# Kernel tuning notes

Hardware: AMD Instinct MI355X
Metric: run time of the kernel (lower is better)

The kernel has to match this reference:

```python
import jax, jax.numpy as jnp
import numpy as np

B, S, D, H, DH = 2, 2048, 1024, 16, 64
GLOBAL_RATIO = 0.1
LN_EPS = 1e-5


def setup_inputs() -> dict:
    key = jax.random.key(0)
    ks = jax.random.split(key, 8)
    w = lambda k, shape: jax.random.normal(k, shape, jnp.float32) * 0.02
    return {
        'x': jax.random.normal(ks[0], (B, S, D), jnp.float32),
        'Wq': w(ks[1], (D, H * DH)),
        'Wk': w(ks[2], (D, H * DH)),
        'Wv': w(ks[3], (D, H * DH)),
        'Wo': w(ks[4], (H * DH, D)),
        'bo': jnp.zeros((D,), jnp.float32),
        'ln_gamma': jnp.ones((DH,), jnp.float32),
        'ln_beta': jnp.zeros((DH,), jnp.float32),
        'Wg': w(ks[5], (2 * DH, DH)),
        'bg': jnp.zeros((DH,), jnp.float32),
    }


def _layernorm(x, gamma, beta):
    mu = jnp.mean(x, axis=-1, keepdims=True)
    var = jnp.mean(jnp.square(x - mu), axis=-1, keepdims=True)
    return (x - mu) * jax.lax.rsqrt(var + LN_EPS) * gamma + beta


def reference(x, Wq, Wk, Wv, Wo, bo, ln_gamma, ln_beta, Wg, bg):
    b, s, _ = x.shape
    # projections -> [b, h, n, d]
    split = lambda t: t.reshape(b, s, H, DH).transpose(0, 2, 1, 3)
    q = split(x @ Wq)
    k = split(x @ Wk)
    v = split(x @ Wv)
    scale = DH ** -0.5

    # local (full) attention: manual QK^T / softmax / AV
    scores = jnp.einsum('bhnd,bhmd->bhnm', q, k) * scale  # [b,h,s,s]
    attn = jax.nn.softmax(scores, axis=-1)
    local_out = jnp.einsum('bhnm,bhmd->bhnd', attn, v)

    # cross-segment fusion: top-k keys by norm per (b, h)
    num_global = max(1, int(s * GLOBAL_RATIO))
    key_norms = jnp.linalg.norm(k, axis=-1)  # [b,h,s]
    _, top_idx = jax.lax.top_k(key_norms, num_global)  # [b,h,g]
    idx = top_idx[..., None]  # [b,h,g,1]
    global_k = jnp.take_along_axis(k, idx, axis=2)  # [b,h,g,d]
    global_v = jnp.take_along_axis(v, idx, axis=2)
    g_scores = jnp.einsum('bhnd,bhgd->bhng', q, global_k) * scale
    g_attn = jax.nn.softmax(g_scores, axis=-1)
    global_out = jnp.einsum('bhng,bhgd->bhnd', g_attn, global_v)
    global_out = _layernorm(global_out, ln_gamma, ln_beta)

    # learned gate over [local, global]
    cat = jnp.concatenate([local_out, global_out], axis=-1)  # [b,h,s,2d]
    gate = jax.nn.sigmoid(cat @ Wg + bg)
    fused = gate * local_out + (1.0 - gate) * global_out

    out = fused.transpose(0, 2, 1, 3).reshape(b, s, H * DH)  # b h n d -> b n (h d)
    return out @ Wo + bo
```

## Files before the change

### kernel.cpp

```cpp
#include <hip/hip_runtime.h>


constexpr int SEQ    = 2048;
constexpr int DMODEL = 1024;
constexpr int NH     = 16;
constexpr int DHEAD  = 64;
constexpr int BHT    = 32;
constexpr int NG     = 204;
constexpr int NGPAD  = 256;
constexpr float LNEPS = 1e-5f;

typedef __attribute__((ext_vector_type(8))) short short8;
typedef __attribute__((ext_vector_type(4))) short short4v;
typedef __attribute__((ext_vector_type(4))) float f32x4;

__device__ __forceinline__ unsigned short f2bf(float f) {
    unsigned int u = __float_as_uint(f);
    u += 0x7FFFu + ((u >> 16) & 1u);
    return (unsigned short)(u >> 16);
}
__device__ __forceinline__ float bf2f(unsigned short b) {
    return __uint_as_float(((unsigned int)b) << 16);
}

__global__ __launch_bounds__(256)
void prep_k(const float* __restrict__ x,
            const float* __restrict__ Wq, const float* __restrict__ Wv,
            const float* __restrict__ Wo, const float* __restrict__ Wk,
            const float* __restrict__ Wg,
            unsigned short* __restrict__ xh, unsigned short* __restrict__ xl,
            unsigned short* __restrict__ Wqt, unsigned short* __restrict__ Wvt,
            unsigned short* __restrict__ Wot, unsigned short* __restrict__ Wkh,
            unsigned short* __restrict__ Wkl, unsigned short* __restrict__ Wgt)
{
    const int bid = blockIdx.x;
    const int tid = threadIdx.x;

    if (bid < 2048) {
        int i = (bid * 256 + tid) << 3;
        short8 h, l;
#pragma unroll
        for (int j = 0; j < 8; ++j) {
            float v = x[i + j];
            unsigned short hb = f2bf(v);
            h[j] = (short)hb;
            l[j] = (short)f2bf(v - bf2f(hb));
        }
        *(short8*)(xh + i) = h;
        *(short8*)(xl + i) = l;
        return;
    }
    if (bid == 3072) {
#pragma unroll
        for (int i = 0; i < 32; ++i) {
            int o = tid * 32 + i;
            int dg = o >> 7, jj = o & 127;
            Wgt[o] = f2bf(Wg[jj * 64 + dg]);
        }
        return;
    }

    __shared__ float tile[64][68];
    const int sub = bid - 2048;
    const int which = sub >> 8;
    const int b = sub & 255;
    const int n0 = (b & 15) * 64, k0 = (b >> 4) * 64;
    const float* W = (which == 0) ? Wq : (which == 1) ? Wv : (which == 2) ? Wo : Wk;
    const int Kd = DMODEL, Nd = DMODEL;

#pragma unroll
    for (int p = 0; p < 4; ++p) {
        int c = tid + (p << 8);
        int r = c >> 4, c4 = (c & 15) << 2;
        *(float4*)&tile[r][c4] = *(const float4*)(W + (size_t)(k0 + r) * Nd + n0 + c4);
    }
    __syncthreads();
#pragma unroll
    for (int p = 0; p < 4; ++p) {
        int c = tid + (p << 8);
        int n = c >> 4, k4 = (c & 15) << 2;
        if (which < 3) {
            unsigned short* Wt = (which == 0) ? Wqt : (which == 1) ? Wvt : Wot;
            short4v o;
#pragma unroll
            for (int j = 0; j < 4; ++j) o[j] = (short)f2bf(tile[k4 + j][n]);
            *(short4v*)(Wt + (size_t)(n0 + n) * Kd + k0 + k4) = o;
        } else {
            short4v oh, ol;
#pragma unroll
            for (int j = 0; j < 4; ++j) {
                float v = tile[k4 + j][n];
                unsigned short hb = f2bf(v);
                oh[j] = (short)hb;
                ol[j] = (short)f2bf(v - bf2f(hb));
            }
            *(short4v*)(Wkh + (size_t)(n0 + n) * Kd + k0 + k4) = oh;
            *(short4v*)(Wkl + (size_t)(n0 + n) * Kd + k0 + k4) = ol;
        }
    }
}

__global__ __launch_bounds__(512)
void gemm_bf16_k(const unsigned short* __restrict__ A,
                 const unsigned short* __restrict__ Bt,
                 const float* __restrict__ bias,
                 void* __restrict__ outv, void* __restrict__ outv2,
                 unsigned short* __restrict__ vtout,
                 int M, int N, int K, int mode)
{
    __shared__ __align__(16) unsigned short As[128][72];
    __shared__ __align__(16) unsigned short Bs[128][72];
    const int tid = threadIdx.x;
    const int lane = tid & 63, wave = tid >> 6;
    const int quad = lane >> 4, ln = lane & 15;
    const int mh = (wave >> 2) << 6;
    const int nh = (wave & 3) << 5;
    const int m0 = blockIdx.y * 128, n0 = blockIdx.x * 128;

    f32x4 acc[4][2];
#pragma unroll
    for (int i = 0; i < 4; ++i)
#pragma unroll
        for (int j = 0; j < 2; ++j) acc[i][j] = (f32x4){0.f, 0.f, 0.f, 0.f};

    short8 areg[2], breg[2];
#pragma unroll
    for (int p = 0; p < 2; ++p) {
        int c = tid + (p << 9);
        int row = c >> 3, col8 = (c & 7) << 3;
        areg[p] = *(const short8*)(A + (size_t)(m0 + row) * K + col8);
        breg[p] = *(const short8*)(Bt + (size_t)(n0 + row) * K + col8);
    }

    for (int k0 = 0; k0 < K; k0 += 64) {
        __syncthreads();
#pragma unroll
        for (int p = 0; p < 2; ++p) {
            int c = tid + (p << 9);
            int row = c >> 3, col8 = (c & 7) << 3;
            *(short8*)&As[row][col8] = areg[p];
            *(short8*)&Bs[row][col8] = breg[p];
        }
        __syncthreads();
        if (k0 + 64 < K) {
#pragma unroll
            for (int p = 0; p < 2; ++p) {
                int c = tid + (p << 9);
                int row = c >> 3, col8 = (c & 7) << 3;
                areg[p] = *(const short8*)(A + (size_t)(m0 + row) * K + k0 + 64 + col8);
                breg[p] = *(const short8*)(Bt + (size_t)(n0 + row) * K + k0 + 64 + col8);
            }
        }
#pragma unroll
        for (int ch = 0; ch < 2; ++ch) {
            short8 af[4], bf[2];
#pragma unroll
            for (int mt = 0; mt < 4; ++mt)
                af[mt] = *(const short8*)&As[mh + mt * 16 + ln][ch * 32 + quad * 8];
#pragma unroll
            for (int nt = 0; nt < 2; ++nt)
                bf[nt] = *(const short8*)&Bs[nh + nt * 16 + ln][ch * 32 + quad * 8];
#pragma unroll
            for (int mt = 0; mt < 4; ++mt)
#pragma unroll
                for (int nt = 0; nt < 2; ++nt)
                    acc[mt][nt] = __builtin_amdgcn_mfma_f32_16x16x32_bf16(
                        af[mt], bf[nt], acc[mt][nt], 0, 0, 0);
        }
    }

    if (mode == 0) {
        float* out = (float*)outv;
#pragma unroll
        for (int mt = 0; mt < 4; ++mt)
#pragma unroll
            for (int nt = 0; nt < 2; ++nt)
#pragma unroll
                for (int r = 0; r < 4; ++r) {
                    int m = m0 + mh + mt * 16 + quad * 4 + r;
                    int n = n0 + nh + nt * 16 + ln;
                    out[(size_t)m * N + n] = acc[mt][nt][r] + bias[n];
                }
    } else {
#pragma unroll
        for (int mt = 0; mt < 4; ++mt)
#pragma unroll
            for (int nt = 0; nt < 2; ++nt) {
                int n = n0 + nh + nt * 16 + ln;
                int mb = m0 + mh + mt * 16 + quad * 4;
                int b = mb >> 11, s0 = mb & (SEQ - 1);
                int d = n & 63;
                if (n < DMODEL) {
                    int h = n >> 6;
                    unsigned short* qp_ =
                        (unsigned short*)outv + ((size_t)(b * NH + h) * SEQ + s0) * DHEAD + d;
#pragma unroll
                    for (int r = 0; r < 4; ++r)
                        qp_[(size_t)r * DHEAD] = f2bf(acc[mt][nt][r] * 0.18033688f);
                } else {
                    int h = (n >> 6) - NH;
                    unsigned short* vp_ =
                        (unsigned short*)outv2 + ((size_t)(b * NH + h) * SEQ + s0) * DHEAD + d;
                    short4v tv;
#pragma unroll
                    for (int r = 0; r < 4; ++r) {
                        unsigned short bv = f2bf(acc[mt][nt][r]);
                        vp_[(size_t)r * DHEAD] = bv;
                        tv[r] = (short)bv;
                    }
                    *(short4v*)(vtout + ((size_t)(b * NH + h) * DHEAD + d) * SEQ + s0) = tv;
                }
            }
    }
}

__global__ __launch_bounds__(512)
void gemm_kproj_mfma(const unsigned short* __restrict__ xh,
                     const unsigned short* __restrict__ xl,
                     const unsigned short* __restrict__ Wh,
                     const unsigned short* __restrict__ Wl,
                     unsigned short* __restrict__ kout,
                     float* __restrict__ norms2)
{
    __shared__ __align__(16) unsigned short Ah[64][72];
    __shared__ __align__(16) unsigned short Al[64][72];
    __shared__ __align__(16) unsigned short Bh[128][72];
    __shared__ __align__(16) unsigned short Bl[128][72];
    const int K = DMODEL;
    const int tid = threadIdx.x;
    const int lane = tid & 63, wave = tid >> 6;
    const int quad = lane >> 4, ln = lane & 15;
    const int mh = (wave >> 1) << 4;
    const int nh = (wave & 1) << 6;
    const int m0 = blockIdx.y * 64, n0 = blockIdx.x * 128;

    f32x4 acc[4];
#pragma unroll
    for (int j = 0; j < 4; ++j) acc[j] = (f32x4){0.f, 0.f, 0.f, 0.f};

    const int arow = tid >> 3, acol8 = (tid & 7) << 3;
    short8 ahreg, alreg, bhreg[2], blreg[2];
    {
        size_t ga = (size_t)(m0 + arow) * K + acol8;
        ahreg = *(const short8*)(xh + ga);
        alreg = *(const short8*)(xl + ga);
#pragma unroll
        for (int p = 0; p < 2; ++p) {
            int c = tid + (p << 9);
            int row = c >> 3, col8 = (c & 7) << 3;
            size_t gb = (size_t)(n0 + row) * K + col8;
            bhreg[p] = *(const short8*)(Wh + gb);
            blreg[p] = *(const short8*)(Wl + gb);
        }
    }

    for (int k0 = 0; k0 < K; k0 += 64) {
        __syncthreads();
        *(short8*)&Ah[arow][acol8] = ahreg;
        *(short8*)&Al[arow][acol8] = alreg;
#pragma unroll
        for (int p = 0; p < 2; ++p) {
            int c = tid + (p << 9);
            int row = c >> 3, col8 = (c & 7) << 3;
            *(short8*)&Bh[row][col8] = bhreg[p];
            *(short8*)&Bl[row][col8] = blreg[p];
        }
        __syncthreads();
        if (k0 + 64 < K) {
            size_t ga = (size_t)(m0 + arow) * K + k0 + 64 + acol8;
            ahreg = *(const short8*)(xh + ga);
            alreg = *(const short8*)(xl + ga);
#pragma unroll
            for (int p = 0; p < 2; ++p) {
                int c = tid + (p << 9);
                int row = c >> 3, col8 = (c & 7) << 3;
                size_t gb = (size_t)(n0 + row) * K + k0 + 64 + col8;
                bhreg[p] = *(const short8*)(Wh + gb);
                blreg[p] = *(const short8*)(Wl + gb);
            }
        }
#pragma unroll
        for (int ch = 0; ch < 2; ++ch) {
            short8 bh4[4], bl4[4];
#pragma unroll
            for (int nt = 0; nt < 4; ++nt) {
                bh4[nt] = *(const short8*)&Bh[nh + nt * 16 + ln][ch * 32 + quad * 8];
                bl4[nt] = *(const short8*)&Bl[nh + nt * 16 + ln][ch * 32 + quad * 8];
            }
            short8 ah = *(const short8*)&Ah[mh + ln][ch * 32 + quad * 8];
            short8 al = *(const short8*)&Al[mh + ln][ch * 32 + quad * 8];
#pragma unroll
            for (int nt = 0; nt < 4; ++nt) {
                acc[nt] = __builtin_amdgcn_mfma_f32_16x16x32_bf16(ah, bh4[nt], acc[nt], 0, 0, 0);
                acc[nt] = __builtin_amdgcn_mfma_f32_16x16x32_bf16(ah, bl4[nt], acc[nt], 0, 0, 0);
                acc[nt] = __builtin_amdgcn_mfma_f32_16x16x32_bf16(al, bh4[nt], acc[nt], 0, 0, 0);
            }
        }
    }

    const int h = (n0 + nh) >> 6;
#pragma unroll
    for (int r = 0; r < 4; ++r) {
        int m = m0 + mh + quad * 4 + r;
        int b = m >> 11, s = m & (SEQ - 1);
        size_t rowbase = ((size_t)(b * NH + h) * SEQ + s) * DHEAD;
#pragma unroll
        for (int nt = 0; nt < 4; ++nt)
            kout[rowbase + nt * 16 + ln] = f2bf(acc[nt][r]);
        float s2 = acc[0][r] * acc[0][r] + acc[1][r] * acc[1][r] +
                   acc[2][r] * acc[2][r] + acc[3][r] * acc[3][r];
#pragma unroll
        for (int off = 1; off <= 8; off <<= 1)
            s2 += __shfl_xor(s2, off);
        if (ln == 0)
            norms2[(size_t)(b * NH + h) * SEQ + s] = s2;
    }
}

__global__ __launch_bounds__(512)
void topk_gather_k(const float* __restrict__ norms2,
                   const unsigned short* __restrict__ k,
                   const unsigned short* __restrict__ v,
                   unsigned short* __restrict__ gk,
                   unsigned short* __restrict__ gvt)
{
    __shared__ unsigned long long keys[SEQ];
    __shared__ int tix[NGPAD];
    __shared__ __align__(16) unsigned short T[64][72];
    const int bh = blockIdx.x;
    const int tid = threadIdx.x;
    const float* nb = norms2 + (size_t)bh * SEQ;
    const size_t base = (size_t)bh * SEQ * DHEAD;

    for (int i = tid; i < SEQ; i += 512) {
        float nrm = sqrtf(nb[i]);
        keys[i] = ((unsigned long long)__float_as_uint(nrm) << 32) |
                  (unsigned int)(0xFFFFFFFFu - (unsigned int)i);
    }
    __syncthreads();
    for (int kk = 2; kk <= SEQ; kk <<= 1) {
        for (int j = kk >> 1; j > 0; j >>= 1) {
            for (int i = tid; i < SEQ; i += 512) {
                int ixj = i ^ j;
                if (ixj > i) {
                    unsigned long long a = keys[i], b = keys[ixj];
                    bool up = ((i & kk) == 0);
                    if ((a > b) == up) { keys[i] = b; keys[ixj] = a; }
                }
            }
            __syncthreads();
        }
    }
    if (tid < NGPAD) {
        tix[tid] = (tid < NG)
            ? (int)(0xFFFFFFFFu - (unsigned int)(keys[SEQ - 1 - tid] & 0xFFFFFFFFu))
            : 0;
    }
    __syncthreads();

    for (int t = 0; t < NGPAD / 64; ++t) {
        {
            int idx = tid;
            int row = idx >> 3, col8 = (idx & 7) << 3;
            int g = t * 64 + row;
            short8 kv = (short8)0, vv = (short8)0;
            if (g < NG) {
                int sidx = tix[g];
                kv = *(const short8*)(k + base + (size_t)sidx * DHEAD + col8);
                vv = *(const short8*)(v + base + (size_t)sidx * DHEAD + col8);
            }
            *(short8*)(gk + ((size_t)bh * NGPAD + g) * DHEAD + col8) = kv;
            *(short8*)&T[row][col8] = vv;
        }
        __syncthreads();
        {
            int idx = tid;
            int d = idx >> 3, k8 = (idx & 7) << 3;
            short8 o;
#pragma unroll
            for (int i = 0; i < 8; ++i) o[i] = (short)T[k8 + i][d];
            *(short8*)(gvt + ((size_t)bh * DHEAD + d) * NGPAD + t * 64 + k8) = o;
        }
        __syncthreads();
    }
}

__global__ __launch_bounds__(256, 2)
void attn_fused_k(const unsigned short* __restrict__ qb,
                  const unsigned short* __restrict__ kb,
                  const unsigned short* __restrict__ vt,
                  const unsigned short* __restrict__ gk,
                  const unsigned short* __restrict__ gvt,
                  const unsigned short* __restrict__ Wgt,
                  const float* __restrict__ gamma,
                  const float* __restrict__ beta,
                  const float* __restrict__ bg,
                  unsigned short* __restrict__ fused)
{
    __shared__ __align__(16) unsigned short smem[27136];
    unsigned short* const KsB = smem;
    unsigned short* const VtB = smem + 9216;
    unsigned short (*Ps)[72]  = (unsigned short (*)[72])smem;
    unsigned short (*Wgs)[136] = (unsigned short (*)[136])(smem + 18432);

    const int flat = blockIdx.x;
    const int bh = ((flat >> 7) << 3) | (flat & 7);
    const int q0 = ((flat >> 3) & 15) * 128;
    const int tid = threadIdx.x;
    const int lane = tid & 63, wave = tid >> 6;
    const int quad = lane >> 4, ln = lane & 15;
    const size_t base = (size_t)bh * SEQ * DHEAD;
    const unsigned short* gkb = gk + (size_t)bh * NGPAD * DHEAD;
    const unsigned short* gvb = gvt + (size_t)bh * DHEAD * NGPAD;

#pragma unroll
    for (int p = 0; p < 4; ++p) {
        int idx = tid + (p << 8);
        *(short8*)&Wgs[idx >> 4][(idx & 15) << 3] = *(const short8*)(Wgt + idx * 8);
    }

    short8 qf[2][2];
#pragma unroll
    for (int mt = 0; mt < 2; ++mt) {
        const unsigned short* qp = qb + base + (size_t)(q0 + wave * 32 + mt * 16 + ln) * DHEAD;
        qf[mt][0] = *(const short8*)(qp + quad * 8);
        qf[mt][1] = *(const short8*)(qp + 32 + quad * 8);
    }

    f32x4 O[2][4], Og[2][4];
#pragma unroll
    for (int mt = 0; mt < 2; ++mt)
#pragma unroll
        for (int nt = 0; nt < 4; ++nt) {
            O[mt][nt] = (f32x4){0.f, 0.f, 0.f, 0.f};
            Og[mt][nt] = (f32x4){0.f, 0.f, 0.f, 0.f};
        }
    float ls[2] = {0.f, 0.f}, lg[2] = {0.f, 0.f};

    short8 kreg[2], vreg[2];
    int srow[2], scol8[2];
#pragma unroll
    for (int p = 0; p < 2; ++p) {
        int idx = tid + (p << 8);
        srow[p] = idx >> 3;
        scol8[p] = (idx & 7) << 3;
    }

    auto loadT = [&](int i) {
#pragma unroll
        for (int p = 0; p < 2; ++p) {
            if (i < 32) {
                kreg[p] = *(const short8*)(kb + base + (size_t)(i * 64 + srow[p]) * DHEAD + scol8[p]);
                vreg[p] = *(const short8*)(vt + base + (size_t)srow[p] * SEQ + i * 64 + scol8[p]);
            } else {
                int g = i - 32;
                kreg[p] = *(const short8*)(gkb + (size_t)(g * 64 + srow[p]) * DHEAD + scol8[p]);
                vreg[p] = *(const short8*)(gvb + (size_t)srow[p] * NGPAD + g * 64 + scol8[p]);
            }
        }
    };
    auto storeT = [&](int buf) {
        unsigned short* kd = KsB + buf * 4608;
        unsigned short* vd = VtB + buf * 4608;
#pragma unroll
        for (int p = 0; p < 2; ++p) {
            *(short8*)&kd[srow[p] * 72 + scol8[p]] = kreg[p];
            *(short8*)&vd[srow[p] * 72 + scol8[p]] = vreg[p];
        }
    };

    loadT(0);
    storeT(0);
    loadT(1);
    __syncthreads();

    for (int t = 0; t < 32; ++t) {
        const int cur = t & 1;
        const unsigned short* Kc = KsB + cur * 4608;
        const unsigned short* Vc = VtB + cur * 4608;

        f32x4 s[2][4];
#pragma unroll
        for (int mt = 0; mt < 2; ++mt)
#pragma unroll
            for (int nt = 0; nt < 4; ++nt) s[mt][nt] = (f32x4){0.f, 0.f, 0.f, 0.f};
        __builtin_amdgcn_s_setprio(1);
#pragma unroll
        for (int nt = 0; nt < 4; ++nt) {
            short8 kf0 = *(const short8*)&Kc[(nt * 16 + ln) * 72 + quad * 8];
            short8 kf1 = *(const short8*)&Kc[(nt * 16 + ln) * 72 + 32 + quad * 8];
#pragma unroll
            for (int mt = 0; mt < 2; ++mt) {
                s[mt][nt] = __builtin_amdgcn_mfma_f32_16x16x32_bf16(kf0, qf[mt][0], s[mt][nt], 0, 0, 0);
                s[mt][nt] = __builtin_amdgcn_mfma_f32_16x16x32_bf16(kf1, qf[mt][1], s[mt][nt], 0, 0, 0);
            }
        }
        __builtin_amdgcn_s_setprio(0);

        short4v pf[2][4];
#pragma unroll
        for (int mt = 0; mt < 2; ++mt)
#pragma unroll
            for (int nt = 0; nt < 4; ++nt)
#pragma unroll
                for (int r = 0; r < 4; ++r) {
                    unsigned int u = __float_as_uint(__builtin_amdgcn_exp2f(s[mt][nt][r]));
                    ls[mt] += __uint_as_float(u & 0xFFFF0000u);
                    pf[mt][nt][r] = (short)(u >> 16);
                }

        __builtin_amdgcn_s_setprio(1);
#pragma unroll
        for (int dt = 0; dt < 4; ++dt)
#pragma unroll
            for (int ks = 0; ks < 4; ++ks) {
                short4v vf = *(const short4v*)&Vc[(dt * 16 + ln) * 72 + ks * 16 + quad * 4];
#pragma unroll
                for (int mt = 0; mt < 2; ++mt)
                    O[mt][dt] = __builtin_amdgcn_mfma_f32_16x16x16bf16_1k(
                        pf[mt][ks], vf, O[mt][dt], 0, 0, 0);
            }
        __builtin_amdgcn_s_setprio(0);

        storeT(cur ^ 1);
        if (t + 2 <= 35) loadT(t + 2);
        __syncthreads();
    }

    for (int tg = 0; tg < 4; ++tg) {
        const int t = 32 + tg;
        const int cur = t & 1;
        const unsigned short* Kc = KsB + cur * 4608;
        const unsigned short* Vc = VtB + cur * 4608;

        f32x4 s[2][4];
#pragma unroll
        for (int mt = 0; mt < 2; ++mt)
#pragma unroll
            for (int nt = 0; nt < 4; ++nt) s[mt][nt] = (f32x4){0.f, 0.f, 0.f, 0.f};
        __builtin_amdgcn_s_setprio(1);
#pragma unroll
        for (int nt = 0; nt < 4; ++nt) {
            short8 kf0 = *(const short8*)&Kc[(nt * 16 + ln) * 72 + quad * 8];
            short8 kf1 = *(const short8*)&Kc[(nt * 16 + ln) * 72 + 32 + quad * 8];
#pragma unroll
            for (int mt = 0; mt < 2; ++mt) {
                s[mt][nt] = __builtin_amdgcn_mfma_f32_16x16x32_bf16(kf0, qf[mt][0], s[mt][nt], 0, 0, 0);
                s[mt][nt] = __builtin_amdgcn_mfma_f32_16x16x32_bf16(kf1, qf[mt][1], s[mt][nt], 0, 0, 0);
            }
        }
        __builtin_amdgcn_s_setprio(0);

        short4v pf[2][4];
#pragma unroll
        for (int nt = 0; nt < 4; ++nt)
#pragma unroll
            for (int r = 0; r < 4; ++r) {
                bool valid = (tg * 64 + nt * 16 + quad * 4 + r) < NG;
#pragma unroll
                for (int mt = 0; mt < 2; ++mt) {
                    float p = valid ? __builtin_amdgcn_exp2f(s[mt][nt][r]) : 0.f;
                    unsigned int u = __float_as_uint(p);
                    lg[mt] += __uint_as_float(u & 0xFFFF0000u);
                    pf[mt][nt][r] = (short)(u >> 16);
                }
            }

        __builtin_amdgcn_s_setprio(1);
#pragma unroll
        for (int dt = 0; dt < 4; ++dt)
#pragma unroll
            for (int ks = 0; ks < 4; ++ks) {
                short4v vf = *(const short4v*)&Vc[(dt * 16 + ln) * 72 + ks * 16 + quad * 4];
#pragma unroll
                for (int mt = 0; mt < 2; ++mt)
                    Og[mt][dt] = __builtin_amdgcn_mfma_f32_16x16x16bf16_1k(
                        pf[mt][ks], vf, Og[mt][dt], 0, 0, 0);
            }
        __builtin_amdgcn_s_setprio(0);

        if (t < 35) storeT(cur ^ 1);
        if (t + 2 <= 35) loadT(t + 2);
        __syncthreads();
    }

#pragma unroll
    for (int mt = 0; mt < 2; ++mt) {
        ls[mt] += __shfl_xor(ls[mt], 16);
        ls[mt] += __shfl_xor(ls[mt], 32);
        lg[mt] += __shfl_xor(lg[mt], 16);
        lg[mt] += __shfl_xor(lg[mt], 32);
    }
    float invl[2][4], invg[2][4];
#pragma unroll
    for (int mt = 0; mt < 2; ++mt)
#pragma unroll
        for (int r = 0; r < 4; ++r) {
            invl[mt][r] = 1.f / __shfl(ls[mt], quad * 4 + r);
            invg[mt][r] = 1.f / __shfl(lg[mt], quad * 4 + r);
        }

    float xs[2][4][4];
#pragma unroll
    for (int mt = 0; mt < 2; ++mt)
#pragma unroll
        for (int r = 0; r < 4; ++r) {
            float inv = invg[mt][r];
#pragma unroll
            for (int nt = 0; nt < 4; ++nt) xs[mt][nt][r] = Og[mt][nt][r] * inv;
        }
    float mu[2][4], rsd[2][4];
#pragma unroll
    for (int mt = 0; mt < 2; ++mt)
#pragma unroll
        for (int r = 0; r < 4; ++r) {
            float sm = xs[mt][0][r] + xs[mt][1][r] + xs[mt][2][r] + xs[mt][3][r];
#pragma unroll
            for (int off = 1; off <= 8; off <<= 1) sm += __shfl_xor(sm, off);
            mu[mt][r] = sm * (1.f / 64.f);
        }
#pragma unroll
    for (int mt = 0; mt < 2; ++mt)
#pragma unroll
        for (int r = 0; r < 4; ++r) {
            float sv = 0.f;
#pragma unroll
            for (int nt = 0; nt < 4; ++nt) {
                float d = xs[mt][nt][r] - mu[mt][r];
                sv += d * d;
            }
#pragma unroll
            for (int off = 1; off <= 8; off <<= 1) sv += __shfl_xor(sv, off);
            rsd[mt][r] = rsqrtf(sv * (1.f / 64.f) + LNEPS);
        }
#pragma unroll
    for (int nt = 0; nt < 4; ++nt) {
        float g = gamma[nt * 16 + ln], bb = beta[nt * 16 + ln];
#pragma unroll
        for (int mt = 0; mt < 2; ++mt)
#pragma unroll
            for (int r = 0; r < 4; ++r)
                xs[mt][nt][r] = (xs[mt][nt][r] - mu[mt][r]) * rsd[mt][r] * g + bb;
    }

    float lf[2][4][4];
#pragma unroll
    for (int mt = 0; mt < 2; ++mt)
#pragma unroll
        for (int nt = 0; nt < 4; ++nt)
#pragma unroll
            for (int r = 0; r < 4; ++r) {
                lf[mt][nt][r] = O[mt][nt][r] * invl[mt][r];
                Ps[wave * 32 + mt * 16 + quad * 4 + r][nt * 16 + ln] = f2bf(lf[mt][nt][r]);
            }
    f32x4 gacc[2][4];
#pragma unroll
    for (int ng = 0; ng < 4; ++ng) {
        float bgv = bg[ng * 16 + ln];
#pragma unroll
        for (int mt = 0; mt < 2; ++mt)
            gacc[mt][ng] = (f32x4){bgv, bgv, bgv, bgv};
    }
#pragma unroll
    for (int ch = 0; ch < 2; ++ch) {
        short8 af[2];
#pragma unroll
        for (int mt = 0; mt < 2; ++mt)
            af[mt] = *(const short8*)&Ps[wave * 32 + mt * 16 + ln][ch * 32 + quad * 8];
#pragma unroll
        for (int ng = 0; ng < 4; ++ng) {
            short8 bf = *(const short8*)&Wgs[ng * 16 + ln][ch * 32 + quad * 8];
#pragma unroll
            for (int mt = 0; mt < 2; ++mt)
                gacc[mt][ng] = __builtin_amdgcn_mfma_f32_16x16x32_bf16(af[mt], bf, gacc[mt][ng], 0, 0, 0);
        }
    }
#pragma unroll
    for (int mt = 0; mt < 2; ++mt)
#pragma unroll
        for (int nt = 0; nt < 4; ++nt)
#pragma unroll
            for (int r = 0; r < 4; ++r)
                Ps[wave * 32 + mt * 16 + quad * 4 + r][nt * 16 + ln] = f2bf(xs[mt][nt][r]);
#pragma unroll
    for (int ch = 0; ch < 2; ++ch) {
        short8 af[2];
#pragma unroll
        for (int mt = 0; mt < 2; ++mt)
            af[mt] = *(const short8*)&Ps[wave * 32 + mt * 16 + ln][ch * 32 + quad * 8];
#pragma unroll
        for (int ng = 0; ng < 4; ++ng) {
            short8 bf = *(const short8*)&Wgs[ng * 16 + ln][64 + ch * 32 + quad * 8];
#pragma unroll
            for (int mt = 0; mt < 2; ++mt)
                gacc[mt][ng] = __builtin_amdgcn_mfma_f32_16x16x32_bf16(af[mt], bf, gacc[mt][ng], 0, 0, 0);
        }
    }

    const int b = bh >> 4, h = bh & 15;
#pragma unroll
    for (int mt = 0; mt < 2; ++mt)
#pragma unroll
        for (int ng = 0; ng < 4; ++ng)
#pragma unroll
            for (int r = 0; r < 4; ++r) {
                float gt = 1.f / (1.f + __expf(-gacc[mt][ng][r]));
                float f = gt * lf[mt][ng][r] + (1.f - gt) * xs[mt][ng][r];
                int s = q0 + wave * 32 + mt * 16 + quad * 4 + r;
                fused[((size_t)(b * SEQ + s)) * DMODEL + h * DHEAD + ng * 16 + ln] = f2bf(f);
            }
}

extern "C" void kernel_launch(void* const* d_in, const int* in_sizes, int n_in,
                              void* d_out, int out_size, void* d_ws, size_t ws_size,
                              hipStream_t stream)
{
    (void)in_sizes; (void)n_in; (void)out_size; (void)ws_size;
    const float* x    = (const float*)d_in[0];
    const float* Wq   = (const float*)d_in[1];
    const float* Wk   = (const float*)d_in[2];
    const float* Wv   = (const float*)d_in[3];
    const float* Wo   = (const float*)d_in[4];
    const float* bo   = (const float*)d_in[5];
    const float* ln_g = (const float*)d_in[6];
    const float* ln_b = (const float*)d_in[7];
    const float* Wg   = (const float*)d_in[8];
    const float* bg   = (const float*)d_in[9];

    char* w = (char*)d_ws;
    const size_t MB = 1024ull * 1024ull;
    unsigned short* kb16  = (unsigned short*)(w);
    unsigned short* qb16  = (unsigned short*)(w + 8 * MB);
    unsigned short* vb16  = (unsigned short*)(w + 16 * MB);
    unsigned short* vt16  = (unsigned short*)(w + 24 * MB);
    unsigned short* xh    = (unsigned short*)(w + 32 * MB);
    unsigned short* xl    = (unsigned short*)(w + 40 * MB);
    unsigned short* Wqt   = (unsigned short*)(w + 48 * MB);
    unsigned short* Wvt   = (unsigned short*)(w + 50 * MB);
    unsigned short* Wot   = (unsigned short*)(w + 52 * MB);
    unsigned short* Wkh   = (unsigned short*)(w + 54 * MB);
    unsigned short* Wkl   = (unsigned short*)(w + 56 * MB);
    unsigned short* Wgt   = (unsigned short*)(w + 58 * MB);
    float*          norms2= (float*)(w + 59 * MB);
    unsigned short* gk16  = (unsigned short*)(w + 60 * MB);
    unsigned short* gvt16 = (unsigned short*)(w + 61 * MB);
    unsigned short* fusedb = xh;

    const int M = 4096, N = 1024, K = 1024;

    prep_k<<<3073, 256, 0, stream>>>(x, Wq, Wv, Wo, Wk, Wg,
                                     xh, xl, Wqt, Wvt, Wot, Wkh, Wkl, Wgt);

    dim3 gqv(2048 / 128, M / 128);
    gemm_bf16_k<<<gqv, 512, 0, stream>>>(xh, Wqt, nullptr, qb16, vb16, vt16,
                                         M, 2048, K, 3);

    dim3 gkp(N / 128, M / 64);
    gemm_kproj_mfma<<<gkp, 512, 0, stream>>>(xh, xl, Wkh, Wkl, kb16, norms2);

    topk_gather_k<<<BHT, 512, 0, stream>>>(norms2, kb16, vb16, gk16, gvt16);

    attn_fused_k<<<512, 256, 0, stream>>>(qb16, kb16, vt16, gk16, gvt16, Wgt,
                                          ln_g, ln_b, bg, fusedb);

    dim3 go_(N / 128, M / 128);
    gemm_bf16_k<<<go_, 512, 0, stream>>>(fusedb, Wot, bo, (float*)d_out, nullptr,
                                         nullptr, M, N, K, 0);
}
```

Baseline: 274.9 us.

## Split attention key range across two wave groups per block and merge partials

The attention kernel now runs 512 threads per block. Two halves of four waves each process 18 of the 36 key tiles (32 local plus 4 global), so the sequential KV loop per block is halved. Half 0 writes its partial local output and row sums to shared memory, and half 1 merges them and runs the LayerNorm and gate epilogue. The PV step moves from the 16x16x16 to the 16x16x32 MFMA by permuting K rows on load, and Wg is read from global memory instead of being staged in LDS. The costs are more LDS, a merge barrier, half the threads sitting idle during the epilogue, and possibly lower occupancy from the new launch bounds.

```diff
diff --git a/kernel.cpp b/kernel.cpp
--- a/kernel.cpp
+++ b/kernel.cpp
@@ -385,7 +385,7 @@
     }
 }
 
-__global__ __launch_bounds__(256, 2)
+__global__ __launch_bounds__(512, 4)
 void attn_fused_k(const unsigned short* __restrict__ qb,
                   const unsigned short* __restrict__ kb,
                   const unsigned short* __restrict__ vt,
@@ -397,32 +397,29 @@
                   const float* __restrict__ bg,
                   unsigned short* __restrict__ fused)
 {
-    __shared__ __align__(16) unsigned short smem[27136];
-    unsigned short* const KsB = smem;
-    unsigned short* const VtB = smem + 9216;
-    unsigned short (*Ps)[72]  = (unsigned short (*)[72])smem;
-    unsigned short (*Wgs)[136] = (unsigned short (*)[136])(smem + 18432);
+    __shared__ __align__(16) unsigned short smem[36864];
 
     const int flat = blockIdx.x;
     const int bh = ((flat >> 7) << 3) | (flat & 7);
     const int q0 = ((flat >> 3) & 15) * 128;
     const int tid = threadIdx.x;
     const int lane = tid & 63, wave = tid >> 6;
+    const int half = wave >> 2, w4 = wave & 3;
     const int quad = lane >> 4, ln = lane & 15;
     const size_t base = (size_t)bh * SEQ * DHEAD;
     const unsigned short* gkb = gk + (size_t)bh * NGPAD * DHEAD;
     const unsigned short* gvb = gvt + (size_t)bh * DHEAD * NGPAD;
 
-#pragma unroll
-    for (int p = 0; p < 4; ++p) {
-        int idx = tid + (p << 8);
-        *(short8*)&Wgs[idx >> 4][(idx & 15) << 3] = *(const short8*)(Wgt + idx * 8);
-    }
+    unsigned short* const myKs = smem + half * 9216;
+    unsigned short* const myVt = smem + 18432 + half * 9216;
+    float* const CombO = (float*)smem;
+    float* const ls0f  = (float*)smem + 8320;
+    unsigned short (*Ps)[72] = (unsigned short (*)[72])(smem + 16896);
 
     short8 qf[2][2];
 #pragma unroll
     for (int mt = 0; mt < 2; ++mt) {
-        const unsigned short* qp = qb + base + (size_t)(q0 + wave * 32 + mt * 16 + ln) * DHEAD;
+        const unsigned short* qp = qb + base + (size_t)(q0 + w4 * 32 + mt * 16 + ln) * DHEAD;
         qf[mt][0] = *(const short8*)(qp + quad * 8);
         qf[mt][1] = *(const short8*)(qp + 32 + quad * 8);
     }
@@ -437,31 +434,36 @@
         }
     float ls[2] = {0.f, 0.f}, lg[2] = {0.f, 0.f};
 
+    const int tid_h = tid & 255;
     short8 kreg[2], vreg[2];
-    int srow[2], scol8[2];
+    int srow[2], scol8[2], psrow[2];
 #pragma unroll
     for (int p = 0; p < 2; ++p) {
-        int idx = tid + (p << 8);
+        int idx = tid_h + (p << 8);
         srow[p] = idx >> 3;
         scol8[p] = (idx & 7) << 3;
-    }
-
-    auto loadT = [&](int i) {
+        psrow[p] = (srow[p] & 0x20) | ((srow[p] & 0x0C) << 1) |
+                   ((srow[p] & 0x10) >> 2) | (srow[p] & 3);
+    }
+
+    const int T0 = half * 18;
+
+    auto loadT = [&](int T) {
 #pragma unroll
         for (int p = 0; p < 2; ++p) {
-            if (i < 32) {
-                kreg[p] = *(const short8*)(kb + base + (size_t)(i * 64 + srow[p]) * DHEAD + scol8[p]);
-                vreg[p] = *(const short8*)(vt + base + (size_t)srow[p] * SEQ + i * 64 + scol8[p]);
+            if (T < 32) {
+                kreg[p] = *(const short8*)(kb + base + (size_t)(T * 64 + psrow[p]) * DHEAD + scol8[p]);
+                vreg[p] = *(const short8*)(vt + base + (size_t)srow[p] * SEQ + T * 64 + scol8[p]);
             } else {
-                int g = i - 32;
-                kreg[p] = *(const short8*)(gkb + (size_t)(g * 64 + srow[p]) * DHEAD + scol8[p]);
+                int g = T - 32;
+                kreg[p] = *(const short8*)(gkb + (size_t)(g * 64 + psrow[p]) * DHEAD + scol8[p]);
                 vreg[p] = *(const short8*)(gvb + (size_t)srow[p] * NGPAD + g * 64 + scol8[p]);
             }
         }
     };
     auto storeT = [&](int buf) {
-        unsigned short* kd = KsB + buf * 4608;
-        unsigned short* vd = VtB + buf * 4608;
+        unsigned short* kd = myKs + buf * 4608;
+        unsigned short* vd = myVt + buf * 4608;
 #pragma unroll
         for (int p = 0; p < 2; ++p) {
             *(short8*)&kd[srow[p] * 72 + scol8[p]] = kreg[p];
@@ -469,15 +471,16 @@
         }
     };
 
-    loadT(0);
+    loadT(T0);
     storeT(0);
-    loadT(1);
+    loadT(T0 + 1);
     __syncthreads();
 
-    for (int t = 0; t < 32; ++t) {
-        const int cur = t & 1;
-        const unsigned short* Kc = KsB + cur * 4608;
-        const unsigned short* Vc = VtB + cur * 4608;
+    for (int i = 0; i < 18; ++i) {
+        const int T = T0 + i;
+        const int cur = i & 1;
+        const unsigned short* Kc = myKs + cur * 4608;
+        const unsigned short* Vc = myVt + cur * 4608;
 
         f32x4 s[2][4];
 #pragma unroll
@@ -497,90 +500,64 @@
         }
         __builtin_amdgcn_s_setprio(0);
 
-        short4v pf[2][4];
-#pragma unroll
-        for (int mt = 0; mt < 2; ++mt)
+        short8 pf8[2][2];
+        if (T < 32) {
+#pragma unroll
+            for (int mt = 0; mt < 2; ++mt)
+#pragma unroll
+                for (int nt = 0; nt < 4; ++nt)
+#pragma unroll
+                    for (int r = 0; r < 4; ++r) {
+                        unsigned int u = __float_as_uint(__builtin_amdgcn_exp2f(s[mt][nt][r]));
+                        ls[mt] += __uint_as_float(u & 0xFFFF0000u);
+                        pf8[mt][nt >> 1][((nt & 1) << 2) | r] = (short)(u >> 16);
+                    }
+            __builtin_amdgcn_s_setprio(1);
+#pragma unroll
+            for (int dt = 0; dt < 4; ++dt)
+#pragma unroll
+                for (int c = 0; c < 2; ++c) {
+                    short8 vf = *(const short8*)&Vc[(dt * 16 + ln) * 72 + c * 32 + quad * 8];
+#pragma unroll
+                    for (int mt = 0; mt < 2; ++mt)
+                        O[mt][dt] = __builtin_amdgcn_mfma_f32_16x16x32_bf16(
+                            pf8[mt][c], vf, O[mt][dt], 0, 0, 0);
+                }
+            __builtin_amdgcn_s_setprio(0);
+        } else {
+            const int tg = T - 32;
 #pragma unroll
             for (int nt = 0; nt < 4; ++nt)
 #pragma unroll
                 for (int r = 0; r < 4; ++r) {
-                    unsigned int u = __float_as_uint(__builtin_amdgcn_exp2f(s[mt][nt][r]));
-                    ls[mt] += __uint_as_float(u & 0xFFFF0000u);
-                    pf[mt][nt][r] = (short)(u >> 16);
+                    int phi = ((nt >> 1) << 5) | (quad << 3) | ((nt & 1) << 2) | r;
+                    bool valid = (tg * 64 + phi) < NG;
+#pragma unroll
+                    for (int mt = 0; mt < 2; ++mt) {
+                        float p = valid ? __builtin_amdgcn_exp2f(s[mt][nt][r]) : 0.f;
+                        unsigned int u = __float_as_uint(p);
+                        lg[mt] += __uint_as_float(u & 0xFFFF0000u);
+                        pf8[mt][nt >> 1][((nt & 1) << 2) | r] = (short)(u >> 16);
+                    }
                 }
-
-        __builtin_amdgcn_s_setprio(1);
-#pragma unroll
-        for (int dt = 0; dt < 4; ++dt)
-#pragma unroll
-            for (int ks = 0; ks < 4; ++ks) {
-                short4v vf = *(const short4v*)&Vc[(dt * 16 + ln) * 72 + ks * 16 + quad * 4];
-#pragma unroll
-                for (int mt = 0; mt < 2; ++mt)
-                    O[mt][dt] = __builtin_amdgcn_mfma_f32_16x16x16bf16_1k(
-                        pf[mt][ks], vf, O[mt][dt], 0, 0, 0);
-            }
-        __builtin_amdgcn_s_setprio(0);
-
-        storeT(cur ^ 1);
-        if (t + 2 <= 35) loadT(t + 2);
-        __syncthreads();
-    }
-
-    for (int tg = 0; tg < 4; ++tg) {
-        const int t = 32 + tg;
-        const int cur = t & 1;
-        const unsigned short* Kc = KsB + cur * 4608;
-        const unsigned short* Vc = VtB + cur * 4608;
-
-        f32x4 s[2][4];
-#pragma unroll
-        for (int mt = 0; mt < 2; ++mt)
-#pragma unroll
-            for (int nt = 0; nt < 4; ++nt) s[mt][nt] = (f32x4){0.f, 0.f, 0.f, 0.f};
-        __builtin_amdgcn_s_setprio(1);
-#pragma unroll
-        for (int nt = 0; nt < 4; ++nt) {
-            short8 kf0 = *(const short8*)&Kc[(nt * 16 + ln) * 72 + quad * 8];
-            short8 kf1 = *(const short8*)&Kc[(nt * 16 + ln) * 72 + 32 + quad * 8];
-#pragma unroll
-            for (int mt = 0; mt < 2; ++mt) {
-                s[mt][nt] = __builtin_amdgcn_mfma_f32_16x16x32_bf16(kf0, qf[mt][0], s[mt][nt], 0, 0, 0);
-                s[mt][nt] = __builtin_amdgcn_mfma_f32_16x16x32_bf16(kf1, qf[mt][1], s[mt][nt], 0, 0, 0);
-            }
-        }
-        __builtin_amdgcn_s_setprio(0);
-
-        short4v pf[2][4];
-#pragma unroll
-        for (int nt = 0; nt < 4; ++nt)
-#pragma unroll
-            for (int r = 0; r < 4; ++r) {
-                bool valid = (tg * 64 + nt * 16 + quad * 4 + r) < NG;
-#pragma unroll
-                for (int mt = 0; mt < 2; ++mt) {
-                    float p = valid ? __builtin_amdgcn_exp2f(s[mt][nt][r]) : 0.f;
-                    unsigned int u = __float_as_uint(p);
-                    lg[mt] += __uint_as_float(u & 0xFFFF0000u);
-                    pf[mt][nt][r] = (short)(u >> 16);
+            __builtin_amdgcn_s_setprio(1);
+#pragma unroll
+            for (int dt = 0; dt < 4; ++dt)
+#pragma unroll
+                for (int c = 0; c < 2; ++c) {
+                    short8 vf = *(const short8*)&Vc[(dt * 16 + ln) * 72 + c * 32 + quad * 8];
+#pragma unroll
+                    for (int mt = 0; mt < 2; ++mt)
+                        Og[mt][dt] = __builtin_amdgcn_mfma_f32_16x16x32_bf16(
+                            pf8[mt][c], vf, Og[mt][dt], 0, 0, 0);
                 }
-            }
-
-        __builtin_amdgcn_s_setprio(1);
-#pragma unroll
-        for (int dt = 0; dt < 4; ++dt)
-#pragma unroll
-            for (int ks = 0; ks < 4; ++ks) {
-                short4v vf = *(const short4v*)&Vc[(dt * 16 + ln) * 72 + ks * 16 + quad * 4];
-#pragma unroll
-                for (int mt = 0; mt < 2; ++mt)
-                    Og[mt][dt] = __builtin_amdgcn_mfma_f32_16x16x16bf16_1k(
-                        pf[mt][ks], vf, Og[mt][dt], 0, 0, 0);
-            }
-        __builtin_amdgcn_s_setprio(0);
-
-        if (t < 35) storeT(cur ^ 1);
-        if (t + 2 <= 35) loadT(t + 2);
+            __builtin_amdgcn_s_setprio(0);
+        }
+
+        if (i < 17) {
+            storeT(cur ^ 1);
+            if (i < 16) loadT(T0 + i + 2);
+        }
         __syncthreads();
     }
 
@@ -591,12 +568,41 @@
         lg[mt] += __shfl_xor(lg[mt], 16);
         lg[mt] += __shfl_xor(lg[mt], 32);
     }
+
+    if (half == 0) {
+#pragma unroll
+        for (int mt = 0; mt < 2; ++mt)
+#pragma unroll
+            for (int dt = 0; dt < 4; ++dt)
+#pragma unroll
+                for (int r = 0; r < 4; ++r)
+                    CombO[(size_t)(w4 * 32 + mt * 16 + quad * 4 + r) * 65 + dt * 16 + ln] =
+                        O[mt][dt][r];
+        if (quad == 0) {
+            ls0f[w4 * 32 + ln] = ls[0];
+            ls0f[w4 * 32 + 16 + ln] = ls[1];
+        }
+    }
+    __syncthreads();
+    if (half == 0) return;
+
+    float lsT[2];
+    lsT[0] = ls[0] + ls0f[w4 * 32 + ln];
+    lsT[1] = ls[1] + ls0f[w4 * 32 + 16 + ln];
+#pragma unroll
+    for (int mt = 0; mt < 2; ++mt)
+#pragma unroll
+        for (int dt = 0; dt < 4; ++dt)
+#pragma unroll
+            for (int r = 0; r < 4; ++r)
+                O[mt][dt][r] += CombO[(size_t)(w4 * 32 + mt * 16 + quad * 4 + r) * 65 + dt * 16 + ln];
+
     float invl[2][4], invg[2][4];
 #pragma unroll
     for (int mt = 0; mt < 2; ++mt)
 #pragma unroll
         for (int r = 0; r < 4; ++r) {
-            invl[mt][r] = 1.f / __shfl(ls[mt], quad * 4 + r);
+            invl[mt][r] = 1.f / __shfl(lsT[mt], quad * 4 + r);
             invg[mt][r] = 1.f / __shfl(lg[mt], quad * 4 + r);
         }
 
@@ -651,7 +657,7 @@
 #pragma unroll
             for (int r = 0; r < 4; ++r) {
                 lf[mt][nt][r] = O[mt][nt][r] * invl[mt][r];
-                Ps[wave * 32 + mt * 16 + quad * 4 + r][nt * 16 + ln] = f2bf(lf[mt][nt][r]);
+                Ps[w4 * 32 + mt * 16 + quad * 4 + r][nt * 16 + ln] = f2bf(lf[mt][nt][r]);
             }
     f32x4 gacc[2][4];
 #pragma unroll
@@ -666,10 +672,10 @@
         short8 af[2];
 #pragma unroll
         for (int mt = 0; mt < 2; ++mt)
-            af[mt] = *(const short8*)&Ps[wave * 32 + mt * 16 + ln][ch * 32 + quad * 8];
+            af[mt] = *(const short8*)&Ps[w4 * 32 + mt * 16 + ln][ch * 32 + quad * 8];
 #pragma unroll
         for (int ng = 0; ng < 4; ++ng) {
-            short8 bf = *(const short8*)&Wgs[ng * 16 + ln][ch * 32 + quad * 8];
+            short8 bf = *(const short8*)(Wgt + (size_t)(ng * 16 + ln) * 128 + ch * 32 + quad * 8);
 #pragma unroll
             for (int mt = 0; mt < 2; ++mt)
                 gacc[mt][ng] = __builtin_amdgcn_mfma_f32_16x16x32_bf16(af[mt], bf, gacc[mt][ng], 0, 0, 0);
@@ -681,16 +687,16 @@
         for (int nt = 0; nt < 4; ++nt)
 #pragma unroll
             for (int r = 0; r < 4; ++r)
-                Ps[wave * 32 + mt * 16 + quad * 4 + r][nt * 16 + ln] = f2bf(xs[mt][nt][r]);
+                Ps[w4 * 32 + mt * 16 + quad * 4 + r][nt * 16 + ln] = f2bf(xs[mt][nt][r]);
 #pragma unroll
     for (int ch = 0; ch < 2; ++ch) {
         short8 af[2];
 #pragma unroll
         for (int mt = 0; mt < 2; ++mt)
-            af[mt] = *(const short8*)&Ps[wave * 32 + mt * 16 + ln][ch * 32 + quad * 8];
+            af[mt] = *(const short8*)&Ps[w4 * 32 + mt * 16 + ln][ch * 32 + quad * 8];
 #pragma unroll
         for (int ng = 0; ng < 4; ++ng) {
-            short8 bf = *(const short8*)&Wgs[ng * 16 + ln][64 + ch * 32 + quad * 8];
+            short8 bf = *(const short8*)(Wgt + (size_t)(ng * 16 + ln) * 128 + 64 + ch * 32 + quad * 8);
 #pragma unroll
             for (int mt = 0; mt < 2; ++mt)
                 gacc[mt][ng] = __builtin_amdgcn_mfma_f32_16x16x32_bf16(af[mt], bf, gacc[mt][ng], 0, 0, 0);
@@ -706,7 +712,7 @@
             for (int r = 0; r < 4; ++r) {
                 float gt = 1.f / (1.f + __expf(-gacc[mt][ng][r]));
                 float f = gt * lf[mt][ng][r] + (1.f - gt) * xs[mt][ng][r];
-                int s = q0 + wave * 32 + mt * 16 + quad * 4 + r;
+                int s = q0 + w4 * 32 + mt * 16 + quad * 4 + r;
                 fused[((size_t)(b * SEQ + s)) * DMODEL + h * DHEAD + ng * 16 + ln] = f2bf(f);
             }
 }
@@ -760,7 +766,7 @@
 
     topk_gather_k<<<BHT, 512, 0, stream>>>(norms2, kb16, vb16, gk16, gvt16);
 
-    attn_fused_k<<<512, 256, 0, stream>>>(qb16, kb16, vt16, gk16, gvt16, Wgt,
+    attn_fused_k<<<512, 512, 0, stream>>>(qb16, kb16, vt16, gk16, gvt16, Wgt,
                                           ln_g, ln_b, bg, fusedb);
 
     dim3 go_(N / 128, M / 128);
```

New measurement: 397.1 us. 1.44x slower.

## Use 16x16x32 bf16 MFMA for PV by permuting K rows on load

Applied to the files above, without the earlier changes.

Permutes the order in which K tile rows are loaded into shared memory so that the score MFMA output registers line up with the k-dimension layout of the wider 16x16x32 bf16 MFMA. The P·V product can then use half as many MFMA instructions with 8-element V fragments instead of 16x16x16 with 4-element ones, in both the local and global attention loops. The global-key validity mask is remapped to match the permuted column order. Correctness depends on the row permutation matching the MFMA operand layout exactly.

```diff
diff --git a/kernel.cpp b/kernel.cpp
--- a/kernel.cpp
+++ b/kernel.cpp
@@ -438,23 +438,25 @@
     float ls[2] = {0.f, 0.f}, lg[2] = {0.f, 0.f};
 
     short8 kreg[2], vreg[2];
-    int srow[2], scol8[2];
+    int srow[2], scol8[2], psrow[2];
 #pragma unroll
     for (int p = 0; p < 2; ++p) {
         int idx = tid + (p << 8);
         srow[p] = idx >> 3;
         scol8[p] = (idx & 7) << 3;
+        psrow[p] = (srow[p] & 0x20) | ((srow[p] & 0x0C) << 1) |
+                   ((srow[p] & 0x10) >> 2) | (srow[p] & 3);
     }
 
     auto loadT = [&](int i) {
 #pragma unroll
         for (int p = 0; p < 2; ++p) {
             if (i < 32) {
-                kreg[p] = *(const short8*)(kb + base + (size_t)(i * 64 + srow[p]) * DHEAD + scol8[p]);
+                kreg[p] = *(const short8*)(kb + base + (size_t)(i * 64 + psrow[p]) * DHEAD + scol8[p]);
                 vreg[p] = *(const short8*)(vt + base + (size_t)srow[p] * SEQ + i * 64 + scol8[p]);
             } else {
                 int g = i - 32;
-                kreg[p] = *(const short8*)(gkb + (size_t)(g * 64 + srow[p]) * DHEAD + scol8[p]);
+                kreg[p] = *(const short8*)(gkb + (size_t)(g * 64 + psrow[p]) * DHEAD + scol8[p]);
                 vreg[p] = *(const short8*)(gvb + (size_t)srow[p] * NGPAD + g * 64 + scol8[p]);
             }
         }
@@ -497,7 +499,7 @@
         }
         __builtin_amdgcn_s_setprio(0);
 
-        short4v pf[2][4];
+        short8 pf8[2][2];
 #pragma unroll
         for (int mt = 0; mt < 2; ++mt)
 #pragma unroll
@@ -506,19 +508,19 @@
                 for (int r = 0; r < 4; ++r) {
                     unsigned int u = __float_as_uint(__builtin_amdgcn_exp2f(s[mt][nt][r]));
                     ls[mt] += __uint_as_float(u & 0xFFFF0000u);
-                    pf[mt][nt][r] = (short)(u >> 16);
+                    pf8[mt][nt >> 1][((nt & 1) << 2) | r] = (short)(u >> 16);
                 }
 
         __builtin_amdgcn_s_setprio(1);
 #pragma unroll
         for (int dt = 0; dt < 4; ++dt)
 #pragma unroll
-            for (int ks = 0; ks < 4; ++ks) {
-                short4v vf = *(const short4v*)&Vc[(dt * 16 + ln) * 72 + ks * 16 + quad * 4];
+            for (int c = 0; c < 2; ++c) {
+                short8 vf = *(const short8*)&Vc[(dt * 16 + ln) * 72 + c * 32 + quad * 8];
 #pragma unroll
                 for (int mt = 0; mt < 2; ++mt)
-                    O[mt][dt] = __builtin_amdgcn_mfma_f32_16x16x16bf16_1k(
-                        pf[mt][ks], vf, O[mt][dt], 0, 0, 0);
+                    O[mt][dt] = __builtin_amdgcn_mfma_f32_16x16x32_bf16(
+                        pf8[mt][c], vf, O[mt][dt], 0, 0, 0);
             }
         __builtin_amdgcn_s_setprio(0);
 
@@ -551,18 +553,19 @@
         }
         __builtin_amdgcn_s_setprio(0);
 
-        short4v pf[2][4];
+        short8 pf8[2][2];
 #pragma unroll
         for (int nt = 0; nt < 4; ++nt)
 #pragma unroll
             for (int r = 0; r < 4; ++r) {
-                bool valid = (tg * 64 + nt * 16 + quad * 4 + r) < NG;
+                int phi = ((nt >> 1) << 5) | (quad << 3) | ((nt & 1) << 2) | r;
+                bool valid = (tg * 64 + phi) < NG;
 #pragma unroll
                 for (int mt = 0; mt < 2; ++mt) {
                     float p = valid ? __builtin_amdgcn_exp2f(s[mt][nt][r]) : 0.f;
                     unsigned int u = __float_as_uint(p);
                     lg[mt] += __uint_as_float(u & 0xFFFF0000u);
-                    pf[mt][nt][r] = (short)(u >> 16);
+                    pf8[mt][nt >> 1][((nt & 1) << 2) | r] = (short)(u >> 16);
                 }
             }
 
@@ -570,12 +573,12 @@
 #pragma unroll
         for (int dt = 0; dt < 4; ++dt)
 #pragma unroll
-            for (int ks = 0; ks < 4; ++ks) {
-                short4v vf = *(const short4v*)&Vc[(dt * 16 + ln) * 72 + ks * 16 + quad * 4];
+            for (int c = 0; c < 2; ++c) {
+                short8 vf = *(const short8*)&Vc[(dt * 16 + ln) * 72 + c * 32 + quad * 8];
 #pragma unroll
                 for (int mt = 0; mt < 2; ++mt)
-                    Og[mt][dt] = __builtin_amdgcn_mfma_f32_16x16x16bf16_1k(
-                        pf[mt][ks], vf, Og[mt][dt], 0, 0, 0);
+                    Og[mt][dt] = __builtin_amdgcn_mfma_f32_16x16x32_bf16(
+                        pf8[mt][c], vf, Og[mt][dt], 0, 0, 0);
             }
         __builtin_amdgcn_s_setprio(0);
 
```

Result: faster. 267.8 us (-2.6%).
